# Kernel tuning notes

Measured on AMD Instinct MI355X. Metric: run time of the kernel, lower is better.

The kernel has to match this reference:

```python
import jax, jax.numpy as jnp
import numpy as np

RADIUS = 8          # default radius in refine_mask_with_matting
EPS = 1e-05         # matting_eps
THRESH = 0.8        # threshold


def _box_filter(x, r):
    # F.avg_pool2d(kernel=2r+1, stride=1, padding=r) with count_include_pad=True:
    # zero-padded window sum divided by (2r+1)^2 everywhere (including borders).
    k = 2 * r + 1
    s = jax.lax.reduce_window(
        x, 0.0, jax.lax.add,
        window_dimensions=(1, 1, k, k),
        window_strides=(1, 1, 1, 1),
        padding=((0, 0), (0, 0), (r, r), (r, r)),
    )
    return s / (k * k)


def _guided_filter(guide, src, r, eps):
    # guide, src: [B,1,H,W]
    mean_I = _box_filter(guide, r)
    mean_p = _box_filter(src, r)
    mean_Ip = _box_filter(guide * src, r)
    cov_Ip = mean_Ip - mean_I * mean_p
    mean_II = _box_filter(guide * guide, r)
    var_I = mean_II - mean_I * mean_I
    a = cov_Ip / (var_I + eps)
    b = mean_p - a * mean_I
    mean_a = _box_filter(a, r)
    mean_b = _box_filter(b, r)
    return mean_a * guide + mean_b


def setup_inputs() -> dict:
    key = jax.random.key(0)
    k1, k2 = jax.random.split(key)
    B, C, H, W = 16, 3, 512, 512
    return {
        "output": jax.random.normal(k1, (B, C, H, W), dtype=jnp.float32),
        "input": jax.random.normal(k2, (B, C, H, W), dtype=jnp.float32),
    }


def reference(output, input):
    # --- Algorithm 1: light source map detection ---
    img = jnp.where(input.min() < 0, (input + 1.0) * 0.5, input)      # [B,3,H,W] in [0,1]
    max_intensity = jnp.max(img, axis=1, keepdims=True)                # [B,1,H,W]
    initial_mask = (max_intensity > THRESH).astype(img.dtype)          # [B,1,H,W]

    # matting refinement: guided filter with channel-mean guide (batched over B)
    guide = jnp.mean(img, axis=1, keepdims=True)                       # [B,1,H,W]
    refined = _guided_filter(guide, initial_mask, RADIUS, EPS)
    mask = jnp.clip(refined, 0.0, 1.0)                                 # [B,1,H,W]

    light_source = img * mask                                          # [B,3,H,W]

    # --- Eq. 2: L1 between masked output and light source ---
    output_01 = jnp.where(output.min() < 0, (output + 1.0) * 0.5, output)
    output_light_region = output_01 * mask
    loss = jnp.mean(jnp.abs(output_light_region - light_source))
    return loss
```

## Files before the change

### kernel.cpp

```cpp
#include <hip/hip_runtime.h>
#include <math.h>

#define BNUM 16
#define HNUM 512
#define WNUM 512
#define HW (HNUM*WNUM)
#define NPLANE (BNUM*HW)
#define RR 8
#define KWIN 17
#define EPSF 1e-5f
#define THRESHF 0.8f
#define STRIP 128
#define SEG_AB 32
#define SEG_ML 16
#define RPG 2
#define RAMPG ((2*RR)/RPG)
#define INV_KK (1.0f/289.0f)
#define INV_NUMEL (1.0f/12582912.0f)

__global__ __launch_bounds__(256) void prep_kernel(
        const float* __restrict__ outp, const float* __restrict__ inp,
        float* __restrict__ PI, float* __restrict__ PP, float* __restrict__ PS) {
    int pix = (blockIdx.x * 256 + threadIdx.x) * 4;
    if (pix >= NPLANE) return;
    int b = pix >> 18;
    int r = pix & (HW - 1);
    size_t base = (size_t)b * 3 * HW + r;

    float4 a0 = *(const float4*)(inp + base);
    float4 a1 = *(const float4*)(inp + base + HW);
    float4 a2 = *(const float4*)(inp + base + 2 * HW);
    float4 b0 = *(const float4*)(outp + base);
    float4 b1 = *(const float4*)(outp + base + HW);
    float4 b2 = *(const float4*)(outp + base + 2 * HW);

    float4 I4, P4, S4;
#define DOCOMP(M) { \
    float i0 = (a0.M + 1.f) * 0.5f; \
    float i1 = (a1.M + 1.f) * 0.5f; \
    float i2 = (a2.M + 1.f) * 0.5f; \
    I4.M = (i0 + i1 + i2) * (1.f/3.f); \
    float mx = fmaxf(i0, fmaxf(i1, i2)); \
    P4.M = (mx > THRESHF) ? 1.f : 0.f; \
    S4.M = 0.5f * (fabsf(b0.M - a0.M) + fabsf(b1.M - a1.M) + fabsf(b2.M - a2.M)); \
}
    DOCOMP(x) DOCOMP(y) DOCOMP(z) DOCOMP(w)
#undef DOCOMP

    size_t po = (size_t)b * HW + r;
    *(float4*)(PI + po) = I4;
    *(float4*)(PP + po) = P4;
    *(float4*)(PS + po) = S4;
}

__global__ __launch_bounds__(STRIP) void boxc_ab(
        const float* __restrict__ PI, const float* __restrict__ PP,
        float* __restrict__ PA, float* __restrict__ PB) {
    __shared__ float rowI[RPG][STRIP + 2 * RR];
    __shared__ float rowP[RPG][STRIP + 2 * RR];
    __shared__ float ring[4][KWIN][STRIP];

    int t  = threadIdx.x;
    int x0 = blockIdx.x * STRIP;
    int ys = blockIdx.y * SEG_AB;
    int b  = blockIdx.z;

    const float* Ib = PI + (size_t)b * HW;
    const float* Pb = PP + (size_t)b * HW;
    float* Ab = PA + (size_t)b * HW;
    float* Bb = PB + (size_t)b * HW;

    for (int i = t; i < 4 * KWIN * STRIP; i += STRIP) (&ring[0][0][0])[i] = 0.f;

    int xg  = x0 - RR + t;
    bool xok  = (xg >= 0) && (xg < WNUM);
    int xg2 = x0 - RR + STRIP + t;
    bool x2ok = (t < 2 * RR) && (xg2 < WNUM);

    float vI = 0.f, vP = 0.f, vIp = 0.f, vII = 0.f;
    int slot = 0;

    const int NG = (SEG_AB + 2 * RR) / RPG;

    float pi0[RPG], pp0[RPG], pi1[RPG], pp1[RPG];
#pragma unroll
    for (int r = 0; r < RPG; ++r) {
        pi0[r]=0.f; pp0[r]=0.f; pi1[r]=0.f; pp1[r]=0.f;
        int y = ys - RR + r;
        if (y >= 0 && y < HNUM) {
            size_t ro = (size_t)y * WNUM;
            if (xok)  { pi0[r] = Ib[ro + xg];  pp0[r] = Pb[ro + xg]; }
            if (x2ok) { pi1[r] = Ib[ro + xg2]; pp1[r] = Pb[ro + xg2]; }
        }
    }

    for (int g = 0; g < NG; ++g) {
#pragma unroll
        for (int r = 0; r < RPG; ++r) { rowI[r][t] = pi0[r]; rowP[r][t] = pp0[r]; }
        if (t < 2 * RR) {
#pragma unroll
            for (int r = 0; r < RPG; ++r) { rowI[r][STRIP+t] = pi1[r]; rowP[r][STRIP+t] = pp1[r]; }
        }
#pragma unroll
        for (int r = 0; r < RPG; ++r) { pi0[r]=0.f; pp0[r]=0.f; pi1[r]=0.f; pp1[r]=0.f; }
        if (g + 1 < NG) {
#pragma unroll
            for (int r = 0; r < RPG; ++r) {
                int y = ys - RR + (g + 1) * RPG + r;
                if (y >= 0 && y < HNUM) {
                    size_t ro = (size_t)y * WNUM;
                    if (xok)  { pi0[r] = Ib[ro + xg];  pp0[r] = Pb[ro + xg]; }
                    if (x2ok) { pi1[r] = Ib[ro + xg2]; pp1[r] = Pb[ro + xg2]; }
                }
            }
        }
        __syncthreads();

        bool emit = (g >= RAMPG);
#pragma unroll
        for (int r = 0; r < RPG; ++r) {
            float sI=0.f, sP=0.f, sIp=0.f, sII=0.f;
#pragma unroll
            for (int d = 0; d < KWIN; ++d) {
                float iv = rowI[r][t + d];
                float pv = rowP[r][t + d];
                sI += iv; sP += pv; sIp += iv * pv; sII += iv * iv;
            }
            vI  += sI  - ring[0][slot][t]; ring[0][slot][t] = sI;
            vP  += sP  - ring[1][slot][t]; ring[1][slot][t] = sP;
            vIp += sIp - ring[2][slot][t]; ring[2][slot][t] = sIp;
            vII += sII - ring[3][slot][t]; ring[3][slot][t] = sII;
            slot = (slot + 1 == KWIN) ? 0 : slot + 1;

            if (emit) {
                int k = g * RPG + r;
                int yout = ys + k - 2 * RR;
                float mI  = vI  * INV_KK;
                float mP  = vP  * INV_KK;
                float mIp = vIp * INV_KK;
                float mII = vII * INV_KK;
                float cov = mIp - mI * mP;
                float var = mII - mI * mI;
                float a   = cov / (var + EPSF);
                float bb  = mP - a * mI;
                size_t off = (size_t)yout * WNUM + x0 + t;
                Ab[off] = a;
                Bb[off] = bb;
            }
        }
        __syncthreads();
    }
}

__global__ __launch_bounds__(STRIP) void boxc_mask_loss(
        const float* __restrict__ PA, const float* __restrict__ PB,
        const float* __restrict__ PI, const float* __restrict__ PS,
        float* __restrict__ loss_out) {
    __shared__ float rowA[RPG][STRIP + 2 * RR];
    __shared__ float rowB[RPG][STRIP + 2 * RR];
    __shared__ float ring[2][KWIN][STRIP];
    __shared__ float red[2];

    int t  = threadIdx.x;
    int x0 = blockIdx.x * STRIP;
    int ys = blockIdx.y * SEG_ML;
    int b  = blockIdx.z;

    const float* Ab = PA + (size_t)b * HW;
    const float* Bb = PB + (size_t)b * HW;
    const float* Ib = PI + (size_t)b * HW;
    const float* Sb = PS + (size_t)b * HW;

    for (int i = t; i < 2 * KWIN * STRIP; i += STRIP) (&ring[0][0][0])[i] = 0.f;

    int xg  = x0 - RR + t;
    bool xok  = (xg >= 0) && (xg < WNUM);
    int xg2 = x0 - RR + STRIP + t;
    bool x2ok = (t < 2 * RR) && (xg2 < WNUM);

    float vA = 0.f, vB = 0.f;
    int slot = 0;
    float partial = 0.f;

    const int NG = (SEG_ML + 2 * RR) / RPG;

    float pa0[RPG], pb0[RPG], pa1[RPG], pb1[RPG];
#pragma unroll
    for (int r = 0; r < RPG; ++r) {
        pa0[r]=0.f; pb0[r]=0.f; pa1[r]=0.f; pb1[r]=0.f;
        int y = ys - RR + r;
        if (y >= 0 && y < HNUM) {
            size_t ro = (size_t)y * WNUM;
            if (xok)  { pa0[r] = Ab[ro + xg];  pb0[r] = Bb[ro + xg]; }
            if (x2ok) { pa1[r] = Ab[ro + xg2]; pb1[r] = Bb[ro + xg2]; }
        }
    }

    for (int g = 0; g < NG; ++g) {
#pragma unroll
        for (int r = 0; r < RPG; ++r) { rowA[r][t] = pa0[r]; rowB[r][t] = pb0[r]; }
        if (t < 2 * RR) {
#pragma unroll
            for (int r = 0; r < RPG; ++r) { rowA[r][STRIP+t] = pa1[r]; rowB[r][STRIP+t] = pb1[r]; }
        }
#pragma unroll
        for (int r = 0; r < RPG; ++r) { pa0[r]=0.f; pb0[r]=0.f; pa1[r]=0.f; pb1[r]=0.f; }
        if (g + 1 < NG) {
#pragma unroll
            for (int r = 0; r < RPG; ++r) {
                int y = ys - RR + (g + 1) * RPG + r;
                if (y >= 0 && y < HNUM) {
                    size_t ro = (size_t)y * WNUM;
                    if (xok)  { pa0[r] = Ab[ro + xg];  pb0[r] = Bb[ro + xg]; }
                    if (x2ok) { pa1[r] = Ab[ro + xg2]; pb1[r] = Bb[ro + xg2]; }
                }
            }
        }
        __syncthreads();

        bool emit = (g >= RAMPG);
#pragma unroll
        for (int r = 0; r < RPG; ++r) {
            float sA=0.f, sB=0.f;
#pragma unroll
            for (int d = 0; d < KWIN; ++d) {
                sA += rowA[r][t + d];
                sB += rowB[r][t + d];
            }
            vA += sA - ring[0][slot][t]; ring[0][slot][t] = sA;
            vB += sB - ring[1][slot][t]; ring[1][slot][t] = sB;
            slot = (slot + 1 == KWIN) ? 0 : slot + 1;

            if (emit) {
                int k = g * RPG + r;
                int yout = ys + k - 2 * RR;
                float mA = vA * INV_KK;
                float mB = vB * INV_KK;
                size_t off = (size_t)yout * WNUM + x0 + t;
                float refined = mA * Ib[off] + mB;
                float mask = fminf(fmaxf(refined, 0.f), 1.f);
                partial += mask * Sb[off];
            }
        }
        __syncthreads();
    }

#pragma unroll
    for (int off = 32; off > 0; off >>= 1)
        partial += __shfl_down(partial, off);
    if ((t & 63) == 0) red[t >> 6] = partial;
    __syncthreads();
    if (t == 0) atomicAdd(loss_out, (red[0] + red[1]) * INV_NUMEL);
}

extern "C" void kernel_launch(void* const* d_in, const int* in_sizes, int n_in,
                              void* d_out, int out_size, void* d_ws, size_t ws_size,
                              hipStream_t stream) {
    const float* outp = (const float*)d_in[0];
    const float* inp  = (const float*)d_in[1];

    float* ws = (float*)d_ws;
    float* PI = ws;
    float* PP = ws + (size_t)NPLANE;
    float* PS = ws + (size_t)2 * NPLANE;
    float* PA = ws + (size_t)3 * NPLANE;
    float* PB = ws + (size_t)4 * NPLANE;

    hipMemsetAsync(d_out, 0, sizeof(float), stream);

    prep_kernel<<<NPLANE / (256 * 4), 256, 0, stream>>>(outp, inp, PI, PP, PS);

    dim3 grid_ab(WNUM / STRIP, HNUM / SEG_AB, BNUM);
    boxc_ab<<<grid_ab, STRIP, 0, stream>>>(PI, PP, PA, PB);

    dim3 grid_ml(WNUM / STRIP, HNUM / SEG_ML, BNUM);
    boxc_mask_loss<<<grid_ml, STRIP, 0, stream>>>(PA, PB, PI, PS, (float*)d_out);
}
```

Baseline: 204.0 us.

## Split box filters into separate horizontal and vertical passes via global planes

Restructures the guided filter into four kernels. The horizontal 17-tap sums are computed per row in shared memory and fused into the prep pass, then vertical running sums are taken column-wise from global memory. The same split is applied to the a/b mean filter before the loss. This drops the shared-memory ring buffers and per-row syncs but writes and reads several extra full-size intermediate planes. It falls back to the old path when the workspace is too small.

```diff
diff --git a/kernel.cpp b/kernel.cpp
--- a/kernel.cpp
+++ b/kernel.cpp
@@ -10,13 +10,217 @@
 #define KWIN 17
 #define EPSF 1e-5f
 #define THRESHF 0.8f
+#define INV_KK (1.0f/289.0f)
+#define INV_NUMEL (1.0f/12582912.0f)
+#define YSEG 32
+#define LROW 544
+
+__device__ __forceinline__ int swz(int i) { return i + (i >> 5); }
+
+
+__global__ __launch_bounds__(128) void prep_h(
+        const float* __restrict__ outp, const float* __restrict__ inp,
+        float* __restrict__ PI, float* __restrict__ PS,
+        float* __restrict__ HI, float* __restrict__ HP,
+        float* __restrict__ HIp, float* __restrict__ HII) {
+    __shared__ float LI[LROW], LP[LROW], LIp[LROW], LII[LROW];
+    int t = threadIdx.x;
+    int y = blockIdx.x & (HNUM - 1);
+    int b = blockIdx.x >> 9;
+    int x4 = t << 2;
+
+    size_t rbase = (size_t)b * 3 * HW + (size_t)y * WNUM + x4;
+    float4 a0 = *(const float4*)(inp + rbase);
+    float4 a1 = *(const float4*)(inp + rbase + HW);
+    float4 a2 = *(const float4*)(inp + rbase + 2 * HW);
+    float4 c0 = *(const float4*)(outp + rbase);
+    float4 c1 = *(const float4*)(outp + rbase + HW);
+    float4 c2 = *(const float4*)(outp + rbase + 2 * HW);
+
+    if (t < 8)   { int i = swz(t);        LI[i]=0.f; LP[i]=0.f; LIp[i]=0.f; LII[i]=0.f; }
+    if (t >= 120){ int i = swz(t + 400);  LI[i]=0.f; LP[i]=0.f; LIp[i]=0.f; LII[i]=0.f; }
+
+    float4 I4, S4;
+#pragma unroll
+    for (int j = 0; j < 4; ++j) {
+        float ia = (&a0.x)[j], ib = (&a1.x)[j], ic = (&a2.x)[j];
+        float i0 = (ia + 1.f) * 0.5f;
+        float i1 = (ib + 1.f) * 0.5f;
+        float i2 = (ic + 1.f) * 0.5f;
+        float Iv = (i0 + i1 + i2) * (1.f / 3.f);
+        float pv = (fmaxf(i0, fmaxf(i1, i2)) > THRESHF) ? 1.f : 0.f;
+        (&I4.x)[j] = Iv;
+        (&S4.x)[j] = 0.5f * (fabsf((&c0.x)[j] - ia) + fabsf((&c1.x)[j] - ib) + fabsf((&c2.x)[j] - ic));
+        int ii = swz(x4 + j + 8);
+        LI[ii] = Iv; LP[ii] = pv; LIp[ii] = Iv * pv; LII[ii] = Iv * Iv;
+    }
+
+    size_t po = (size_t)b * HW + (size_t)y * WNUM + x4;
+    *(float4*)(PI + po) = I4;
+    *(float4*)(PS + po) = S4;
+    __syncthreads();
+
+    float sI = 0.f, sP = 0.f, sIp = 0.f, sII = 0.f;
+#pragma unroll
+    for (int d = 0; d < KWIN; ++d) {
+        int ii = swz(x4 + d);
+        sI += LI[ii]; sP += LP[ii]; sIp += LIp[ii]; sII += LII[ii];
+    }
+    float4 oI, oP, oIp, oII;
+    (&oI.x)[0]=sI; (&oP.x)[0]=sP; (&oIp.x)[0]=sIp; (&oII.x)[0]=sII;
+#pragma unroll
+    for (int j = 1; j < 4; ++j) {
+        int im = swz(x4 + j - 1), ip = swz(x4 + j + 16);
+        sI  += LI[ip]  - LI[im];
+        sP  += LP[ip]  - LP[im];
+        sIp += LIp[ip] - LIp[im];
+        sII += LII[ip] - LII[im];
+        (&oI.x)[j]=sI; (&oP.x)[j]=sP; (&oIp.x)[j]=sIp; (&oII.x)[j]=sII;
+    }
+    *(float4*)(HI  + po) = oI;
+    *(float4*)(HP  + po) = oP;
+    *(float4*)(HIp + po) = oIp;
+    *(float4*)(HII + po) = oII;
+}
+
+__global__ __launch_bounds__(128) void v_ab(
+        const float* __restrict__ HI, const float* __restrict__ HP,
+        const float* __restrict__ HIp, const float* __restrict__ HII,
+        float* __restrict__ Pa, float* __restrict__ Pb) {
+    int t  = threadIdx.x;
+    int x  = blockIdx.x * 128 + t;
+    int y0 = blockIdx.y * YSEG;
+    int b  = blockIdx.z;
+    size_t base = (size_t)b * HW + x;
+    const float* hi  = HI  + base;
+    const float* hp  = HP  + base;
+    const float* hip = HIp + base;
+    const float* hii = HII + base;
+    float* pa = Pa + base;
+    float* pb = Pb + base;
+
+    float vI = 0.f, vP = 0.f, vIp = 0.f, vII = 0.f;
+#pragma unroll
+    for (int d = -RR; d <= RR; ++d) {
+        int y = y0 + d;
+        if (y >= 0 && y < HNUM) {
+            size_t o = (size_t)y * WNUM;
+            vI += hi[o]; vP += hp[o]; vIp += hip[o]; vII += hii[o];
+        }
+    }
+#pragma unroll 8
+    for (int k = 0; k < YSEG; ++k) {
+        int y = y0 + k;
+        float mI  = vI  * INV_KK;
+        float mP  = vP  * INV_KK;
+        float mIp = vIp * INV_KK;
+        float mII = vII * INV_KK;
+        float cov = mIp - mI * mP;
+        float var = mII - mI * mI;
+        float a   = cov / (var + EPSF);
+        float bb  = mP - a * mI;
+        size_t o = (size_t)y * WNUM;
+        pa[o] = a;
+        pb[o] = bb;
+        int yp = y + RR + 1, ym = y - RR;
+        if (yp < HNUM) { size_t op = (size_t)yp * WNUM; vI += hi[op]; vP += hp[op]; vIp += hip[op]; vII += hii[op]; }
+        if (ym >= 0)   { size_t om = (size_t)ym * WNUM; vI -= hi[om]; vP -= hp[om]; vIp -= hip[om]; vII -= hii[om]; }
+    }
+}
+
+__global__ __launch_bounds__(128) void h_mask(
+        const float* __restrict__ Pa, const float* __restrict__ Pb,
+        float* __restrict__ Ha, float* __restrict__ Hb) {
+    __shared__ float LA[LROW], LB[LROW];
+    int t = threadIdx.x;
+    int y = blockIdx.x & (HNUM - 1);
+    int b = blockIdx.x >> 9;
+    int x4 = t << 2;
+    size_t po = (size_t)b * HW + (size_t)y * WNUM + x4;
+
+    float4 va = *(const float4*)(Pa + po);
+    float4 vb = *(const float4*)(Pb + po);
+
+    if (t < 8)   { int i = swz(t);       LA[i]=0.f; LB[i]=0.f; }
+    if (t >= 120){ int i = swz(t + 400); LA[i]=0.f; LB[i]=0.f; }
+#pragma unroll
+    for (int j = 0; j < 4; ++j) {
+        int ii = swz(x4 + j + 8);
+        LA[ii] = (&va.x)[j];
+        LB[ii] = (&vb.x)[j];
+    }
+    __syncthreads();
+
+    float sA = 0.f, sB = 0.f;
+#pragma unroll
+    for (int d = 0; d < KWIN; ++d) {
+        int ii = swz(x4 + d);
+        sA += LA[ii]; sB += LB[ii];
+    }
+    float4 oA, oB;
+    (&oA.x)[0]=sA; (&oB.x)[0]=sB;
+#pragma unroll
+    for (int j = 1; j < 4; ++j) {
+        int im = swz(x4 + j - 1), ip = swz(x4 + j + 16);
+        sA += LA[ip] - LA[im];
+        sB += LB[ip] - LB[im];
+        (&oA.x)[j]=sA; (&oB.x)[j]=sB;
+    }
+    *(float4*)(Ha + po) = oA;
+    *(float4*)(Hb + po) = oB;
+}
+
+__global__ __launch_bounds__(128) void v_mask_loss(
+        const float* __restrict__ Ha, const float* __restrict__ Hb,
+        const float* __restrict__ PI, const float* __restrict__ PS,
+        float* __restrict__ loss_out) {
+    __shared__ float red[2];
+    int t  = threadIdx.x;
+    int x  = blockIdx.x * 128 + t;
+    int y0 = blockIdx.y * YSEG;
+    int b  = blockIdx.z;
+    size_t base = (size_t)b * HW + x;
+    const float* ha = Ha + base;
+    const float* hb = Hb + base;
+    const float* pi = PI + base;
+    const float* ps = PS + base;
+
+    float vA = 0.f, vB = 0.f;
+#pragma unroll
+    for (int d = -RR; d <= RR; ++d) {
+        int y = y0 + d;
+        if (y >= 0 && y < HNUM) {
+            size_t o = (size_t)y * WNUM;
+            vA += ha[o]; vB += hb[o];
+        }
+    }
+    float partial = 0.f;
+#pragma unroll 8
+    for (int k = 0; k < YSEG; ++k) {
+        int y = y0 + k;
+        size_t o = (size_t)y * WNUM;
+        float mA = vA * INV_KK;
+        float mB = vB * INV_KK;
+        float refined = mA * pi[o] + mB;
+        float mask = fminf(fmaxf(refined, 0.f), 1.f);
+        partial += mask * ps[o];
+        int yp = y + RR + 1, ym = y - RR;
+        if (yp < HNUM) { size_t op = (size_t)yp * WNUM; vA += ha[op]; vB += hb[op]; }
+        if (ym >= 0)   { size_t om = (size_t)ym * WNUM; vA -= ha[om]; vB -= hb[om]; }
+    }
+#pragma unroll
+    for (int off = 32; off > 0; off >>= 1)
+        partial += __shfl_down(partial, off);
+    if ((t & 63) == 0) red[t >> 6] = partial;
+    __syncthreads();
+    if (t == 0) atomicAdd(loss_out, (red[0] + red[1]) * INV_NUMEL);
+}
+
 #define STRIP 128
 #define SEG_AB 32
 #define SEG_ML 16
 #define RPG 2
 #define RAMPG ((2*RR)/RPG)
-#define INV_KK (1.0f/289.0f)
-#define INV_NUMEL (1.0f/12582912.0f)
 
 __global__ __launch_bounds__(256) void prep_kernel(
         const float* __restrict__ outp, const float* __restrict__ inp,
@@ -26,14 +230,12 @@
     int b = pix >> 18;
     int r = pix & (HW - 1);
     size_t base = (size_t)b * 3 * HW + r;
-
     float4 a0 = *(const float4*)(inp + base);
     float4 a1 = *(const float4*)(inp + base + HW);
     float4 a2 = *(const float4*)(inp + base + 2 * HW);
     float4 b0 = *(const float4*)(outp + base);
     float4 b1 = *(const float4*)(outp + base + HW);
     float4 b2 = *(const float4*)(outp + base + 2 * HW);
-
     float4 I4, P4, S4;
 #define DOCOMP(M) { \
     float i0 = (a0.M + 1.f) * 0.5f; \
@@ -46,7 +248,6 @@
 }
     DOCOMP(x) DOCOMP(y) DOCOMP(z) DOCOMP(w)
 #undef DOCOMP
-
     size_t po = (size_t)b * HW + r;
     *(float4*)(PI + po) = I4;
     *(float4*)(PP + po) = P4;
@@ -59,29 +260,22 @@
     __shared__ float rowI[RPG][STRIP + 2 * RR];
     __shared__ float rowP[RPG][STRIP + 2 * RR];
     __shared__ float ring[4][KWIN][STRIP];
-
     int t  = threadIdx.x;
     int x0 = blockIdx.x * STRIP;
     int ys = blockIdx.y * SEG_AB;
     int b  = blockIdx.z;
-
     const float* Ib = PI + (size_t)b * HW;
     const float* Pb = PP + (size_t)b * HW;
     float* Ab = PA + (size_t)b * HW;
     float* Bb = PB + (size_t)b * HW;
-
     for (int i = t; i < 4 * KWIN * STRIP; i += STRIP) (&ring[0][0][0])[i] = 0.f;
-
     int xg  = x0 - RR + t;
     bool xok  = (xg >= 0) && (xg < WNUM);
     int xg2 = x0 - RR + STRIP + t;
     bool x2ok = (t < 2 * RR) && (xg2 < WNUM);
-
     float vI = 0.f, vP = 0.f, vIp = 0.f, vII = 0.f;
     int slot = 0;
-
     const int NG = (SEG_AB + 2 * RR) / RPG;
-
     float pi0[RPG], pp0[RPG], pi1[RPG], pp1[RPG];
 #pragma unroll
     for (int r = 0; r < RPG; ++r) {
@@ -93,7 +287,6 @@
             if (x2ok) { pi1[r] = Ib[ro + xg2]; pp1[r] = Pb[ro + xg2]; }
         }
     }
-
     for (int g = 0; g < NG; ++g) {
 #pragma unroll
         for (int r = 0; r < RPG; ++r) { rowI[r][t] = pi0[r]; rowP[r][t] = pp0[r]; }
@@ -115,7 +308,6 @@
             }
         }
         __syncthreads();
-
         bool emit = (g >= RAMPG);
 #pragma unroll
         for (int r = 0; r < RPG; ++r) {
@@ -131,7 +323,6 @@
             vIp += sIp - ring[2][slot][t]; ring[2][slot][t] = sIp;
             vII += sII - ring[3][slot][t]; ring[3][slot][t] = sII;
             slot = (slot + 1 == KWIN) ? 0 : slot + 1;
-
             if (emit) {
                 int k = g * RPG + r;
                 int yout = ys + k - 2 * RR;
@@ -160,30 +351,23 @@
     __shared__ float rowB[RPG][STRIP + 2 * RR];
     __shared__ float ring[2][KWIN][STRIP];
     __shared__ float red[2];
-
     int t  = threadIdx.x;
     int x0 = blockIdx.x * STRIP;
     int ys = blockIdx.y * SEG_ML;
     int b  = blockIdx.z;
-
     const float* Ab = PA + (size_t)b * HW;
     const float* Bb = PB + (size_t)b * HW;
     const float* Ib = PI + (size_t)b * HW;
     const float* Sb = PS + (size_t)b * HW;
-
     for (int i = t; i < 2 * KWIN * STRIP; i += STRIP) (&ring[0][0][0])[i] = 0.f;
-
     int xg  = x0 - RR + t;
     bool xok  = (xg >= 0) && (xg < WNUM);
     int xg2 = x0 - RR + STRIP + t;
     bool x2ok = (t < 2 * RR) && (xg2 < WNUM);
-
     float vA = 0.f, vB = 0.f;
     int slot = 0;
     float partial = 0.f;
-
     const int NG = (SEG_ML + 2 * RR) / RPG;
-
     float pa0[RPG], pb0[RPG], pa1[RPG], pb1[RPG];
 #pragma unroll
     for (int r = 0; r < RPG; ++r) {
@@ -195,7 +379,6 @@
             if (x2ok) { pa1[r] = Ab[ro + xg2]; pb1[r] = Bb[ro + xg2]; }
         }
     }
-
     for (int g = 0; g < NG; ++g) {
 #pragma unroll
         for (int r = 0; r < RPG; ++r) { rowA[r][t] = pa0[r]; rowB[r][t] = pb0[r]; }
@@ -217,7 +400,6 @@
             }
         }
         __syncthreads();
-
         bool emit = (g >= RAMPG);
 #pragma unroll
         for (int r = 0; r < RPG; ++r) {
@@ -230,7 +412,6 @@
             vA += sA - ring[0][slot][t]; ring[0][slot][t] = sA;
             vB += sB - ring[1][slot][t]; ring[1][slot][t] = sB;
             slot = (slot + 1 == KWIN) ? 0 : slot + 1;
-
             if (emit) {
                 int k = g * RPG + r;
                 int yout = ys + k - 2 * RR;
@@ -244,7 +425,6 @@
         }
         __syncthreads();
     }
-
 #pragma unroll
     for (int off = 32; off > 0; off >>= 1)
         partial += __shfl_down(partial, off);
@@ -258,21 +438,37 @@
                               hipStream_t stream) {
     const float* outp = (const float*)d_in[0];
     const float* inp  = (const float*)d_in[1];
-
     float* ws = (float*)d_ws;
-    float* PI = ws;
-    float* PP = ws + (size_t)NPLANE;
-    float* PS = ws + (size_t)2 * NPLANE;
-    float* PA = ws + (size_t)3 * NPLANE;
-    float* PB = ws + (size_t)4 * NPLANE;
 
     hipMemsetAsync(d_out, 0, sizeof(float), stream);
 
-    prep_kernel<<<NPLANE / (256 * 4), 256, 0, stream>>>(outp, inp, PI, PP, PS);
-
-    dim3 grid_ab(WNUM / STRIP, HNUM / SEG_AB, BNUM);
-    boxc_ab<<<grid_ab, STRIP, 0, stream>>>(PI, PP, PA, PB);
-
-    dim3 grid_ml(WNUM / STRIP, HNUM / SEG_ML, BNUM);
-    boxc_mask_loss<<<grid_ml, STRIP, 0, stream>>>(PA, PB, PI, PS, (float*)d_out);
-}
+    if (ws_size >= (size_t)8 * NPLANE * sizeof(float)) {
+        float* PI  = ws;
+        float* PS  = ws + (size_t)1 * NPLANE;
+        float* HI  = ws + (size_t)2 * NPLANE;
+        float* HP  = ws + (size_t)3 * NPLANE;
+        float* HIp = ws + (size_t)4 * NPLANE;
+        float* HII = ws + (size_t)5 * NPLANE;
+        float* Pa  = ws + (size_t)6 * NPLANE;
+        float* Pb  = ws + (size_t)7 * NPLANE;
+        float* Ha  = HI;
+        float* Hb  = HP;
+
+        prep_h<<<BNUM * HNUM, 128, 0, stream>>>(outp, inp, PI, PS, HI, HP, HIp, HII);
+        dim3 vg(WNUM / 128, HNUM / YSEG, BNUM);
+        v_ab<<<vg, 128, 0, stream>>>(HI, HP, HIp, HII, Pa, Pb);
+        h_mask<<<BNUM * HNUM, 128, 0, stream>>>(Pa, Pb, Ha, Hb);
+        v_mask_loss<<<vg, 128, 0, stream>>>(Ha, Hb, PI, PS, (float*)d_out);
+    } else {
+        float* PI = ws;
+        float* PP = ws + (size_t)NPLANE;
+        float* PS = ws + (size_t)2 * NPLANE;
+        float* PA = ws + (size_t)3 * NPLANE;
+        float* PB = ws + (size_t)4 * NPLANE;
+        prep_kernel<<<NPLANE / (256 * 4), 256, 0, stream>>>(outp, inp, PI, PP, PS);
+        dim3 grid_ab(WNUM / STRIP, HNUM / SEG_AB, BNUM);
+        boxc_ab<<<grid_ab, STRIP, 0, stream>>>(PI, PP, PA, PB);
+        dim3 grid_ml(WNUM / STRIP, HNUM / SEG_ML, BNUM);
+        boxc_mask_loss<<<grid_ml, STRIP, 0, stream>>>(PA, PB, PI, PS, (float*)d_out);
+    }
+}
```

Result: slower. 225.9 us (+10.7%).
